# Optimization experiments

Hardware: AMD Instinct MI355X
Metric: run time of the kernel (lower is better)

Reference implementation:

```python
import jax, jax.numpy as jnp
import numpy as np

N_NODES = 50000
D = 128
N_POS = 400000
N_NEG = 200000  # N_NODES * neg_k(4)
E = N_POS + N_NEG


def setup_inputs() -> dict:
    key = jax.random.key(0)
    k_x, k_w1, k_w2, k_p = jax.random.split(key, 4)
    x = jax.random.normal(k_x, (N_NODES, D), dtype=jnp.float32)
    # torch nn.Linear params: y = x @ W.T + b
    W1 = jax.random.normal(k_w1, (D, 2 * D), dtype=jnp.float32) * (1.0 / np.sqrt(2 * D))
    b1 = jnp.zeros((D,), dtype=jnp.float32)
    W2 = jax.random.normal(k_w2, (1, D), dtype=jnp.float32) * (1.0 / np.sqrt(D))
    b2 = jnp.zeros((1,), dtype=jnp.float32)
    pairs = jax.random.randint(k_p, (2, E), 0, N_NODES, dtype=jnp.int64)
    labels = jnp.concatenate([jnp.ones((N_POS,), jnp.float32), jnp.zeros((N_NEG,), jnp.float32)])
    return {"x": x, "W1": W1, "b1": b1, "W2": W2, "b2": b2, "labels": labels, "pairs": pairs}


def reference(x, W1, b1, W2, b2, labels, pairs):
    us, vs = pairs[0], pairs[1]
    # edge gather + concat: [E, 2D]
    feats = jnp.concatenate([x[us], x[vs]], axis=-1)
    h = jax.nn.relu(feats @ W1.T + b1)            # [E, D]
    z = (h @ W2.T + b2).ravel()                   # [E] logits
    # binary_cross_entropy_with_logits, mean reduction (numerically stable)
    loss = -jnp.mean(labels * jax.nn.log_sigmoid(z) + (1.0 - labels) * jax.nn.log_sigmoid(-z))
    return loss
```

## Files before the change

### kernel.cpp

```cpp
#include <hip/hip_runtime.h>
#include <hip/hip_fp16.h>

#define D 128
#define TWO_D 256

typedef _Float16 half2v __attribute__((ext_vector_type(2)));
typedef _Float16 half8v __attribute__((ext_vector_type(8)));
typedef float floatx4 __attribute__((ext_vector_type(4)));

__device__ inline unsigned int pkrtz(float a, float b) {
    return __builtin_bit_cast(unsigned int, __builtin_amdgcn_cvt_pkrtz(a, b));
}

__global__ void build_wtf(const float* __restrict__ W1,
                          unsigned short* __restrict__ Wtf) {
    const int id = blockIdx.x * 256 + threadIdx.x;
    const int lane = id & 63, ks = (id >> 6) & 3, t = (id >> 8) & 3, w = id >> 10;
    const int quad = lane >> 4, l16 = lane & 15;
    const int o = w * 64 + t * 16 + l16;
    const float* wrow = (o < D) ? (W1 + (size_t)o * TWO_D)
                                : (W1 + (size_t)(o - D) * TWO_D + D);
    const float* wp = wrow + ks * 32 + quad * 8;
    floatx4 w0 = *(const floatx4*)wp;
    floatx4 w1v = *(const floatx4*)(wp + 4);
    uint4 pk;
    pk.x = pkrtz(w0[0], w0[1]);  pk.y = pkrtz(w0[2], w0[3]);
    pk.z = pkrtz(w1v[0], w1v[1]); pk.w = pkrtz(w1v[2], w1v[3]);
    *(uint4*)(Wtf + (size_t)id * 8) = pk;
}

__global__ __launch_bounds__(256) void gemm_nodes(
        const float* __restrict__ x, const unsigned short* __restrict__ Wtf,
        const float* __restrict__ b1,
        unsigned char* __restrict__ AB, float* __restrict__ out0, int nNodes) {
    const int tid  = threadIdx.x;
    const int wave = tid >> 6, lane = tid & 63;
    const int quad = lane >> 4, l16 = lane & 15;
    const int nb0  = blockIdx.x * 64;

    if (blockIdx.x == 0 && tid == 0) *out0 = 0.f;

    half8v Bf[4][4];
    float bias[4];
#pragma unroll
    for (int t = 0; t < 4; ++t) {
        const int o = wave * 64 + t * 16 + l16;
        bias[t] = (o < D) ? b1[o] : 0.f;
#pragma unroll
        for (int ks = 0; ks < 4; ++ks)
            Bf[t][ks] = *(const half8v*)(Wtf +
                ((size_t)(((wave * 4 + t) * 4 + ks) * 64) + lane) * 8);
    }

    __shared__ __align__(16) unsigned short xs[64][136];
    __shared__ __align__(16) float ct[2][16][260];

#pragma unroll
    for (int i = 0; i < 4; ++i) {
        const int c = tid + 256 * i;
        const int row = c >> 4, col8 = c & 15;
        const int node = nb0 + row;
        const int nc = node < nNodes ? node : nNodes - 1;
        const float* xp = x + (size_t)nc * D + col8 * 8;
        floatx4 v0 = *(const floatx4*)xp;
        floatx4 v1 = *(const floatx4*)(xp + 4);
        uint4 pk;
        pk.x = pkrtz(v0[0], v0[1]);  pk.y = pkrtz(v0[2], v0[3]);
        pk.z = pkrtz(v1[0], v1[1]);  pk.w = pkrtz(v1[2], v1[3]);
        *(uint4*)&xs[row][col8 * 8] = pk;
    }
    __syncthreads();

    const int srow = tid >> 4;
    const int sc8  = tid & 15;

    for (int sub = 0; sub < 4; ++sub) {
        half8v Af[4];
#pragma unroll
        for (int ks = 0; ks < 4; ++ks)
            Af[ks] = *(const half8v*)&xs[sub * 16 + l16][ks * 32 + quad * 8];

        floatx4 acc[4];
#pragma unroll
        for (int t = 0; t < 4; ++t) acc[t] = (floatx4){0.f, 0.f, 0.f, 0.f};
#pragma unroll
        for (int ks = 0; ks < 4; ++ks)
#pragma unroll
            for (int t = 0; t < 4; ++t)
                acc[t] = __builtin_amdgcn_mfma_f32_16x16x32_f16(Af[ks], Bf[t][ks], acc[t], 0, 0, 0);

        float (*cts)[260] = ct[sub & 1];
#pragma unroll
        for (int t = 0; t < 4; ++t) {
            const int o = wave * 64 + t * 16 + l16;
#pragma unroll
            for (int r = 0; r < 4; ++r)
                cts[quad * 4 + r][o] = acc[t][r] + bias[t];
        }
        __syncthreads();

        const int nrow = nb0 + sub * 16 + srow;
        if (nrow < nNodes) {
            floatx4 f0 = *(const floatx4*)&cts[srow][sc8 * 16];
            floatx4 f1 = *(const floatx4*)&cts[srow][sc8 * 16 + 4];
            floatx4 f2 = *(const floatx4*)&cts[srow][sc8 * 16 + 8];
            floatx4 f3 = *(const floatx4*)&cts[srow][sc8 * 16 + 12];
            uint4 o8;
            int d;
            d = __builtin_amdgcn_cvt_pk_fp8_f32(f0[0], f0[1], 0, false);
            d = __builtin_amdgcn_cvt_pk_fp8_f32(f0[2], f0[3], d, true);
            o8.x = (unsigned int)d;
            d = __builtin_amdgcn_cvt_pk_fp8_f32(f1[0], f1[1], 0, false);
            d = __builtin_amdgcn_cvt_pk_fp8_f32(f1[2], f1[3], d, true);
            o8.y = (unsigned int)d;
            d = __builtin_amdgcn_cvt_pk_fp8_f32(f2[0], f2[1], 0, false);
            d = __builtin_amdgcn_cvt_pk_fp8_f32(f2[2], f2[3], d, true);
            o8.z = (unsigned int)d;
            d = __builtin_amdgcn_cvt_pk_fp8_f32(f3[0], f3[1], 0, false);
            d = __builtin_amdgcn_cvt_pk_fp8_f32(f3[2], f3[3], d, true);
            o8.w = (unsigned int)d;
            *(uint4*)(AB + (size_t)nrow * TWO_D + sc8 * 16) = o8;
        }
    }
}

__device__ inline float dot4_fp8(unsigned int wa, unsigned int wb,
                                 unsigned int w2lo, unsigned int w2hi, float z) {
#if __has_builtin(__builtin_amdgcn_cvt_pk_f16_fp8)
    half2v a01 = __builtin_bit_cast(half2v, __builtin_amdgcn_cvt_pk_f16_fp8((short)(wa & 0xffffu)));
    half2v a23 = __builtin_bit_cast(half2v, __builtin_amdgcn_cvt_pk_f16_fp8((short)(wa >> 16)));
    half2v b01 = __builtin_bit_cast(half2v, __builtin_amdgcn_cvt_pk_f16_fp8((short)(wb & 0xffffu)));
    half2v b23 = __builtin_bit_cast(half2v, __builtin_amdgcn_cvt_pk_f16_fp8((short)(wb >> 16)));
    half2v zero = {(_Float16)0, (_Float16)0};
    half2v s01 = __builtin_elementwise_max(a01 + b01, zero);
    half2v s23 = __builtin_elementwise_max(a23 + b23, zero);
    z = __builtin_amdgcn_fdot2(s01, __builtin_bit_cast(half2v, w2lo), z, false);
    z = __builtin_amdgcn_fdot2(s23, __builtin_bit_cast(half2v, w2hi), z, false);
#else
    auto a01 = __builtin_amdgcn_cvt_pk_f32_fp8(wa, false);
    auto a23 = __builtin_amdgcn_cvt_pk_f32_fp8(wa, true);
    auto b01 = __builtin_amdgcn_cvt_pk_f32_fp8(wb, false);
    auto b23 = __builtin_amdgcn_cvt_pk_f32_fp8(wb, true);
    half2v wlo = __builtin_bit_cast(half2v, w2lo);
    half2v whi = __builtin_bit_cast(half2v, w2hi);
    float s0 = fmaxf(a01[0] + b01[0], 0.f), s1 = fmaxf(a01[1] + b01[1], 0.f);
    float s2 = fmaxf(a23[0] + b23[0], 0.f), s3 = fmaxf(a23[1] + b23[1], 0.f);
    z = fmaf(s0, (float)wlo[0], z); z = fmaf(s1, (float)wlo[1], z);
    z = fmaf(s2, (float)whi[0], z); z = fmaf(s3, (float)whi[1], z);
#endif
    return z;
}

__device__ inline float dot16(const uint4& a4, const uint4& b4,
                              const uint4& w2a, const uint4& w2b) {
    float z = 0.f;
    z = dot4_fp8(a4.x, b4.x, w2a.x, w2a.y, z);
    z = dot4_fp8(a4.y, b4.y, w2a.z, w2a.w, z);
    z = dot4_fp8(a4.z, b4.z, w2b.x, w2b.y, z);
    z = dot4_fp8(a4.w, b4.w, w2b.z, w2b.w, z);
    return z;
}

__device__ inline float red8(float z) {
    z += __shfl_xor(z, 4, 8);
    z += __shfl_xor(z, 2, 8);
    z += __shfl_xor(z, 1, 8);
    return z;
}

__device__ inline float bce(float z, float y) {
    const float t = __expf(-fabsf(z));
    return fmaxf(z, 0.f) - z * y + __logf(1.f + t);
}

__global__ __launch_bounds__(256) void edge_loss(
        const unsigned char* __restrict__ AB,
        const int* __restrict__ pairs,
        const float* __restrict__ labels,
        const float* __restrict__ W2,
        const float* __restrict__ b2,
        float* __restrict__ out, int E, float invE) {
    __shared__ unsigned int w2p[64];
    const int tid = threadIdx.x;
    if (tid < 64) {
        float2 w = *(const float2*)(W2 + tid * 2);
        half2v p = { (_Float16)w.x, (_Float16)w.y };
        w2p[tid] = __builtin_bit_cast(unsigned int, p);
    }
    __syncthreads();
    const int l8   = tid & 7;
    const int base = tid & 56;
    const uint4 w2a = *(const uint4*)&w2p[l8 * 8];
    const uint4 w2b = *(const uint4*)&w2p[l8 * 8 + 4];
    const float bb2 = b2[0];

    float acc = 0.f;
    const int group = (blockIdx.x * 256 + tid) >> 3;
    const int e0 = group * 8;
    if (e0 < E) {
        const int el = e0 + l8;
        const int u    = pairs[el];
        const int v    = pairs[E + el];
        const float lab = labels[el];

        uint4 A[8], B[8];
#pragma unroll
        for (int k = 0; k < 8; ++k) {
            const int uk = __shfl(u, base + k, 64);
            const int vk = __shfl(v, base + k, 64);
            A[k] = *(const uint4*)(AB + (size_t)uk * TWO_D + l8 * 16);
            B[k] = *(const uint4*)(AB + (size_t)vk * TWO_D + D + l8 * 16);
        }
#pragma unroll
        for (int k = 0; k < 8; ++k) {
            float z = red8(dot16(A[k], B[k], w2a, w2b)) + bb2;
            const float labk = __shfl(lab, base + k, 64);
            if (l8 == 0) acc += bce(z, labk);
        }
    }

#pragma unroll
    for (int m = 32; m >= 1; m >>= 1) acc += __shfl_xor(acc, m, 64);
    __shared__ float red[4];
    if ((tid & 63) == 0) red[tid >> 6] = acc;
    __syncthreads();
    if (tid == 0)
        atomicAdd(out, (red[0] + red[1] + red[2] + red[3]) * invE);
}

extern "C" void kernel_launch(void* const* d_in, const int* in_sizes, int n_in,
                              void* d_out, int out_size, void* d_ws, size_t ws_size,
                              hipStream_t stream) {
    const float* x      = (const float*)d_in[0];
    const float* W1     = (const float*)d_in[1];
    const float* b1     = (const float*)d_in[2];
    const float* W2     = (const float*)d_in[3];
    const float* b2     = (const float*)d_in[4];
    const float* labels = (const float*)d_in[5];
    const int*   pairs  = (const int*)d_in[6];

    const int nNodes = in_sizes[0] / D;
    const int E      = in_sizes[5];

    unsigned char*  AB  = (unsigned char*)d_ws;
    unsigned short* Wtf = (unsigned short*)((char*)d_ws + 13000704);

    build_wtf<<<16, 256, 0, stream>>>(W1, Wtf);
    gemm_nodes<<<(nNodes + 63) / 64, 256, 0, stream>>>(x, Wtf, b1, AB,
                                                        (float*)d_out, nNodes);
    const int nGroups = (E + 7) / 8;
    const int nBlocks = (nGroups + 31) / 32;
    edge_loss<<<nBlocks, 256, 0, stream>>>(AB, pairs, labels, W2, b2,
                                           (float*)d_out, E, 1.0f / (float)E);
}
```

Measured before the change: 125.8 us.

## Convert edge loss kernel to grid-stride loop with three edges in flight

The edge loss kernel launched one 8-lane group per 8 edges, with shuffled indices and 16 outstanding 16-byte gathers per lane. It now launches a fixed 2048-block grid where each 8-lane group strides over edges, processing three edges per iteration. Each lane loads pair indices and labels directly instead of shuffling them. The goal is fewer blocks, fewer atomics and less register pressure, at the cost of fewer loads in flight per lane (6 instead of 16), which may expose more gather latency.

New measurement: 126.5 us (median of 2 runs). About the same (+0.6%).

```diff
diff --git a/kernel.cpp b/kernel.cpp
--- a/kernel.cpp
+++ b/kernel.cpp
@@ -188,35 +188,42 @@
         w2p[tid] = __builtin_bit_cast(unsigned int, p);
     }
     __syncthreads();
-    const int l8   = tid & 7;
-    const int base = tid & 56;
+    const int l8 = tid & 7;
     const uint4 w2a = *(const uint4*)&w2p[l8 * 8];
     const uint4 w2b = *(const uint4*)&w2p[l8 * 8 + 4];
     const float bb2 = b2[0];
 
     float acc = 0.f;
     const int group = (blockIdx.x * 256 + tid) >> 3;
-    const int e0 = group * 8;
-    if (e0 < E) {
-        const int el = e0 + l8;
-        const int u    = pairs[el];
-        const int v    = pairs[E + el];
-        const float lab = labels[el];
-
-        uint4 A[8], B[8];
-#pragma unroll
-        for (int k = 0; k < 8; ++k) {
-            const int uk = __shfl(u, base + k, 64);
-            const int vk = __shfl(v, base + k, 64);
-            A[k] = *(const uint4*)(AB + (size_t)uk * TWO_D + l8 * 16);
-            B[k] = *(const uint4*)(AB + (size_t)vk * TWO_D + D + l8 * 16);
+    const int S     = (gridDim.x * 256) >> 3;
+
+    int e = group;
+    for (; e + 2 * S < E; e += 3 * S) {
+        const int ea = e, eb = e + S, ec = e + 2 * S;
+        const int ua = pairs[ea], va = pairs[E + ea];
+        const int ub = pairs[eb], vb = pairs[E + eb];
+        const int uc = pairs[ec], vc = pairs[E + ec];
+        uint4 Aa = *(const uint4*)(AB + (size_t)ua * TWO_D + l8 * 16);
+        uint4 Ba = *(const uint4*)(AB + (size_t)va * TWO_D + D + l8 * 16);
+        uint4 Ab = *(const uint4*)(AB + (size_t)ub * TWO_D + l8 * 16);
+        uint4 Bb = *(const uint4*)(AB + (size_t)vb * TWO_D + D + l8 * 16);
+        uint4 Ac = *(const uint4*)(AB + (size_t)uc * TWO_D + l8 * 16);
+        uint4 Bc = *(const uint4*)(AB + (size_t)vc * TWO_D + D + l8 * 16);
+        float za = red8(dot16(Aa, Ba, w2a, w2b)) + bb2;
+        float zb = red8(dot16(Ab, Bb, w2a, w2b)) + bb2;
+        float zc = red8(dot16(Ac, Bc, w2a, w2b)) + bb2;
+        if (l8 == 0) {
+            acc += bce(za, labels[ea]);
+            acc += bce(zb, labels[eb]);
+            acc += bce(zc, labels[ec]);
         }
-#pragma unroll
-        for (int k = 0; k < 8; ++k) {
-            float z = red8(dot16(A[k], B[k], w2a, w2b)) + bb2;
-            const float labk = __shfl(lab, base + k, 64);
-            if (l8 == 0) acc += bce(z, labk);
-        }
+    }
+    for (; e < E; e += S) {
+        const int u = pairs[e], v = pairs[E + e];
+        uint4 A4 = *(const uint4*)(AB + (size_t)u * TWO_D + l8 * 16);
+        uint4 B4 = *(const uint4*)(AB + (size_t)v * TWO_D + D + l8 * 16);
+        float z = red8(dot16(A4, B4, w2a, w2b)) + bb2;
+        if (l8 == 0) acc += bce(z, labels[e]);
     }
 
 #pragma unroll
@@ -248,8 +255,6 @@
     build_wtf<<<16, 256, 0, stream>>>(W1, Wtf);
     gemm_nodes<<<(nNodes + 63) / 64, 256, 0, stream>>>(x, Wtf, b1, AB,
                                                         (float*)d_out, nNodes);
-    const int nGroups = (E + 7) / 8;
-    const int nBlocks = (nGroups + 31) / 32;
-    edge_loss<<<nBlocks, 256, 0, stream>>>(AB, pairs, labels, W2, b2,
-                                           (float*)d_out, E, 1.0f / (float)E);
-}
+    edge_loss<<<2048, 256, 0, stream>>>(AB, pairs, labels, W2, b2,
+                                        (float*)d_out, E, 1.0f / (float)E);
+}
```
